# Performance work log

Measured on AMD Instinct MI355X. Metric: run time of the kernel, lower is better.

Reference implementation:

```python
import jax, jax.numpy as jnp
import numpy as np

N_NODES = 100000
N_EDGES = 1600000
INPUT_DIM = 128
HIDDEN = 128
OUTPUT_DIM = 2
NUM_LAYERS = 2
MAX_RECURSION = 10
TAU_THRESHOLD = 0.005


def setup_inputs() -> dict:
    key = jax.random.key(0)
    ks = jax.random.split(key, 16)
    s = 0.05
    x = jax.random.normal(ks[0], (N_NODES, INPUT_DIM), dtype=jnp.float32)
    edge_index = jax.random.randint(ks[1], (2, N_EDGES), 0, N_NODES, dtype=jnp.int64)
    W_in = jax.random.normal(ks[2], (HIDDEN, INPUT_DIM), dtype=jnp.float32) * s
    b_in = jax.random.normal(ks[3], (HIDDEN,), dtype=jnp.float32) * s
    Wd = jax.random.normal(ks[4], (NUM_LAYERS, HIDDEN, 2 * HIDDEN), dtype=jnp.float32) * s
    bd = jax.random.normal(ks[5], (NUM_LAYERS, HIDDEN), dtype=jnp.float32) * s
    Wt = jax.random.normal(ks[6], (1, HIDDEN), dtype=jnp.float32) * s
    bt = jax.random.normal(ks[7], (1,), dtype=jnp.float32) * s
    W_ih = jax.random.normal(ks[8], (3 * HIDDEN, HIDDEN), dtype=jnp.float32) * s
    W_hh = jax.random.normal(ks[9], (3 * HIDDEN, HIDDEN), dtype=jnp.float32) * s
    b_ih = jax.random.normal(ks[10], (3 * HIDDEN,), dtype=jnp.float32) * s
    b_hh = jax.random.normal(ks[11], (3 * HIDDEN,), dtype=jnp.float32) * s
    Wo = jax.random.normal(ks[12], (OUTPUT_DIM, HIDDEN), dtype=jnp.float32) * s
    bo = jax.random.normal(ks[13], (OUTPUT_DIM,), dtype=jnp.float32) * s
    return dict(x=x, edge_index=edge_index, W_in=W_in, b_in=b_in, Wd=Wd, bd=bd,
                Wt=Wt, bt=bt, W_ih=W_ih, W_hh=W_hh, b_ih=b_ih, b_hh=b_hh, Wo=Wo, bo=bo)


def _gru_cell(x, h, W_ih, W_hh, b_ih, b_hh):
    # torch.nn.GRUCell math
    gi = x @ W_ih.T + b_ih  # [N, 3H]
    gh = h @ W_hh.T + b_hh
    i_r, i_z, i_n = jnp.split(gi, 3, axis=-1)
    h_r, h_z, h_n = jnp.split(gh, 3, axis=-1)
    r = jax.nn.sigmoid(i_r + h_r)
    z = jax.nn.sigmoid(i_z + h_z)
    n = jnp.tanh(i_n + r * h_n)
    return (1.0 - z) * n + z * h


def reference(x, edge_index, W_in, b_in, Wd, bd, Wt, bt, W_ih, W_hh, b_ih, b_hh, Wo, bo):
    N = x.shape[0]
    row, col = edge_index[0], edge_index[1]
    h = jax.nn.relu(x @ W_in.T + b_in)  # [N, H]
    tau = None
    for l in range(NUM_LAYERS):
        diff = jnp.abs(h[row] - h[col])  # [E, H]
        diff_agg = jax.ops.segment_sum(diff, row, num_segments=N)  # [N, H]
        h = jax.nn.relu(jnp.concatenate([h, diff_agg], axis=-1) @ Wd[l].T + bd[l])
        tau = jax.nn.softplus(h @ Wt.T + bt).squeeze(-1)  # [N]
        # n_updates = clamp(floor(1/tau), max=MAX_RECURSION); node updated iff
        # n_updates > 0 and tau < TAU_THRESHOLD. The original inner loop applies
        # gru(diff_agg[i], h[i]) with the ORIGINAL h[i] each iteration, so repeated
        # application is idempotent -> single masked GRU step is exact same math.
        n_updates = jnp.minimum(jnp.floor(1.0 / tau).astype(jnp.int32), MAX_RECURSION)
        mask = (n_updates > 0) & (tau < TAU_THRESHOLD)
        h_gru = _gru_cell(diff_agg, h, W_ih, W_hh, b_ih, b_hh)
        h = jnp.where(mask[:, None], h_gru, h)
    out = h @ Wo.T + bo  # [N, OUTPUT_DIM]
    return out, tau
```

## Files before the change

### kernel.cpp

```cpp
#include <hip/hip_runtime.h>
#include <cstdint>
#include <cstddef>

#define HID 128
#define BSHIFT 7
#define NSB 256
#define MAXB 4096

__global__ __launch_bounds__(256)
void ecount_kernel(const int* __restrict__ row, int* __restrict__ countsT,
                   int E, int nbuck,
                   const float* __restrict__ W_in, const float* __restrict__ Wd,
                   const float* __restrict__ W_ih, const float* __restrict__ W_hh,
                   float* __restrict__ WinT, float* __restrict__ WdT0,
                   float* __restrict__ WdT1, float* __restrict__ WihT,
                   float* __restrict__ WhhT) {
  for (int i = blockIdx.x * 256 + threadIdx.x; i < 180224; i += NSB * 256) {
    int j = i;
    if (j < 16384) { int r = j >> 7, c = j & 127; WinT[c * 128 + r] = W_in[j]; continue; }
    j -= 16384;
    if (j < 32768) { int r = j >> 8, c = j & 255; WdT0[c * 128 + r] = Wd[j]; continue; }
    j -= 32768;
    if (j < 32768) { int r = j >> 8, c = j & 255; WdT1[c * 128 + r] = Wd[32768 + j]; continue; }
    j -= 32768;
    if (j < 49152) { int r = j >> 7, c = j & 127; WihT[c * 384 + r] = W_ih[j]; continue; }
    j -= 49152;
    { int r = j >> 7, c = j & 127; WhhT[c * 384 + r] = W_hh[j]; }
  }
  __shared__ int lh[1024];
  int b = blockIdx.x;
  for (int i = threadIdx.x; i < nbuck; i += 256) lh[i] = 0;
  __syncthreads();
  int per = (E + NSB - 1) / NSB;
  int s = b * per, e = min(s + per, E);
  for (int i = s + (int)threadIdx.x; i < e; i += 256)
    atomicAdd(&lh[row[i] >> BSHIFT], 1);
  __syncthreads();
  for (int i = threadIdx.x; i < nbuck; i += 256) countsT[i * NSB + b] = lh[i];
}

__global__ __launch_bounds__(NSB)
void bprefix_kernel(int* __restrict__ countsT, int* __restrict__ btotal, int nbuck) {
  __shared__ int sd[NSB];
  int bk = blockIdx.x;
  int t = threadIdx.x;
  int v = countsT[bk * NSB + t];
  sd[t] = v;
  __syncthreads();
  for (int off = 1; off < NSB; off <<= 1) {
    int u = (t >= off) ? sd[t - off] : 0;
    __syncthreads();
    sd[t] += u;
    __syncthreads();
  }
  countsT[bk * NSB + t] = sd[t] - v;
  if (t == NSB - 1) btotal[bk] = sd[t];
}

__global__ __launch_bounds__(1024)
void bstart_kernel(const int* __restrict__ btotal, int* __restrict__ bstart,
                   int* __restrict__ offsets, int N, int nbuck) {
  __shared__ int sd[1024];
  int t = threadIdx.x;
  int v = (t < nbuck) ? btotal[t] : 0;
  sd[t] = v;
  __syncthreads();
  for (int off = 1; off < 1024; off <<= 1) {
    int u = (t >= off) ? sd[t - off] : 0;
    __syncthreads();
    sd[t] += u;
    __syncthreads();
  }
  if (t < nbuck) bstart[t] = sd[t] - v;
  if (t == nbuck - 1) { bstart[nbuck] = sd[t]; offsets[N] = sd[t]; }
}

__global__ __launch_bounds__(256)
void escatter_kernel(const int* __restrict__ row, const int* __restrict__ col,
                     const int* __restrict__ countsT, const int* __restrict__ bstart,
                     int2* __restrict__ ebuf, int E, int nbuck) {
  __shared__ int lcur[1024];
  int b = blockIdx.x;
  for (int i = threadIdx.x; i < nbuck; i += 256)
    lcur[i] = bstart[i] + countsT[i * NSB + b];
  __syncthreads();
  int per = (E + NSB - 1) / NSB;
  int s = b * per, e = min(s + per, E);
  for (int i = s + (int)threadIdx.x; i < e; i += 256) {
    int r = row[i], c = col[i];
    int pos = atomicAdd(&lcur[r >> BSHIFT], 1);
    ebuf[pos] = make_int2(r, c);
  }
}

__global__ __launch_bounds__(256)
void bsort_kernel(const int2* __restrict__ ebuf, const int* __restrict__ bstart,
                  int* __restrict__ offsets, int* __restrict__ csr_col,
                  int N, int nbuck) {
  __shared__ int cnt[128], off[128], cur[128];
  __shared__ int lcol[MAXB];
  int bk = blockIdx.x;
  int tid = threadIdx.x;
  int s = bstart[bk], e = bstart[bk + 1];
  int m = e - s;
  if (tid < 128) cnt[tid] = 0;
  __syncthreads();
  for (int i = s + tid; i < e; i += 256)
    atomicAdd(&cnt[ebuf[i].x & 127], 1);
  __syncthreads();
  if (tid < 128) off[tid] = cnt[tid];
  __syncthreads();
  for (int d = 1; d < 128; d <<= 1) {
    int v = 0;
    if (tid < 128 && tid >= d) v = off[tid - d];
    __syncthreads();
    if (tid < 128) off[tid] += v;
    __syncthreads();
  }
  if (tid < 128) {
    cur[tid] = off[tid] - cnt[tid];
    int node = (bk << BSHIFT) + tid;
    if (node < N) offsets[node] = s + off[tid] - cnt[tid];
  }
  __syncthreads();
  if (m <= MAXB) {
    for (int i = s + tid; i < e; i += 256) {
      int2 rc = ebuf[i];
      int pos = atomicAdd(&cur[rc.x & 127], 1);
      lcol[pos] = rc.y;
    }
    __syncthreads();
    if (tid < 128) {
      int b0 = off[tid] - cnt[tid], b1 = off[tid];
      for (int i = b0 + 1; i < b1; ++i) {
        int key = lcol[i];
        int j = i - 1;
        while (j >= b0 && lcol[j] > key) { lcol[j + 1] = lcol[j]; --j; }
        lcol[j + 1] = key;
      }
    }
    __syncthreads();
    for (int i = tid; i < m; i += 256) csr_col[s + i] = lcol[i];
  } else {
    for (int i = s + tid; i < e; i += 256) {
      int2 rc = ebuf[i];
      int pos = atomicAdd(&cur[rc.x & 127], 1);
      csr_col[s + pos] = rc.y;
    }
  }
}

__global__ __launch_bounds__(256)
void aggregate_kernel(const float* __restrict__ h, const int* __restrict__ offsets,
                      const int* __restrict__ csr_col, float* __restrict__ diff,
                      int N) {
  int wave = threadIdx.x >> 6;
  int lane = threadIdx.x & 63;
  int node = blockIdx.x * 4 + wave;
  if (node >= N) return;
  int start = offsets[node], end = offsets[node + 1];
  int deg = end - start;
  const float2* hrow = (const float2*)(h + (size_t)node * HID);
  float2 hv = hrow[lane];
  float a0 = 0.f, a1 = 0.f;

  int batch = min(deg, 64);
  int myc = (lane < batch) ? csr_col[start + lane] : 0;
  int j = 0;
  for (; j + 16 <= batch; j += 16) {
    const float2* p0 = (const float2*)(h + (size_t)__shfl(myc, j + 0) * HID);
    const float2* p1 = (const float2*)(h + (size_t)__shfl(myc, j + 1) * HID);
    const float2* p2 = (const float2*)(h + (size_t)__shfl(myc, j + 2) * HID);
    const float2* p3 = (const float2*)(h + (size_t)__shfl(myc, j + 3) * HID);
    const float2* p4 = (const float2*)(h + (size_t)__shfl(myc, j + 4) * HID);
    const float2* p5 = (const float2*)(h + (size_t)__shfl(myc, j + 5) * HID);
    const float2* p6 = (const float2*)(h + (size_t)__shfl(myc, j + 6) * HID);
    const float2* p7 = (const float2*)(h + (size_t)__shfl(myc, j + 7) * HID);
    const float2* q0 = (const float2*)(h + (size_t)__shfl(myc, j + 8) * HID);
    const float2* q1 = (const float2*)(h + (size_t)__shfl(myc, j + 9) * HID);
    const float2* q2 = (const float2*)(h + (size_t)__shfl(myc, j + 10) * HID);
    const float2* q3 = (const float2*)(h + (size_t)__shfl(myc, j + 11) * HID);
    const float2* q4 = (const float2*)(h + (size_t)__shfl(myc, j + 12) * HID);
    const float2* q5 = (const float2*)(h + (size_t)__shfl(myc, j + 13) * HID);
    const float2* q6 = (const float2*)(h + (size_t)__shfl(myc, j + 14) * HID);
    const float2* q7 = (const float2*)(h + (size_t)__shfl(myc, j + 15) * HID);
    float2 x0 = p0[lane], x1 = p1[lane], x2 = p2[lane], x3 = p3[lane];
    float2 x4 = p4[lane], x5 = p5[lane], x6 = p6[lane], x7 = p7[lane];
    float2 y0 = q0[lane], y1 = q1[lane], y2 = q2[lane], y3 = q3[lane];
    float2 y4 = q4[lane], y5 = q5[lane], y6 = q6[lane], y7 = q7[lane];
    a0 += fabsf(hv.x - x0.x) + fabsf(hv.x - x1.x) + fabsf(hv.x - x2.x) + fabsf(hv.x - x3.x)
        + fabsf(hv.x - x4.x) + fabsf(hv.x - x5.x) + fabsf(hv.x - x6.x) + fabsf(hv.x - x7.x);
    a1 += fabsf(hv.y - x0.y) + fabsf(hv.y - x1.y) + fabsf(hv.y - x2.y) + fabsf(hv.y - x3.y)
        + fabsf(hv.y - x4.y) + fabsf(hv.y - x5.y) + fabsf(hv.y - x6.y) + fabsf(hv.y - x7.y);
    a0 += fabsf(hv.x - y0.x) + fabsf(hv.x - y1.x) + fabsf(hv.x - y2.x) + fabsf(hv.x - y3.x)
        + fabsf(hv.x - y4.x) + fabsf(hv.x - y5.x) + fabsf(hv.x - y6.x) + fabsf(hv.x - y7.x);
    a1 += fabsf(hv.y - y0.y) + fabsf(hv.y - y1.y) + fabsf(hv.y - y2.y) + fabsf(hv.y - y3.y)
        + fabsf(hv.y - y4.y) + fabsf(hv.y - y5.y) + fabsf(hv.y - y6.y) + fabsf(hv.y - y7.y);
  }
  for (; j + 8 <= batch; j += 8) {
    const float2* p0 = (const float2*)(h + (size_t)__shfl(myc, j + 0) * HID);
    const float2* p1 = (const float2*)(h + (size_t)__shfl(myc, j + 1) * HID);
    const float2* p2 = (const float2*)(h + (size_t)__shfl(myc, j + 2) * HID);
    const float2* p3 = (const float2*)(h + (size_t)__shfl(myc, j + 3) * HID);
    const float2* p4 = (const float2*)(h + (size_t)__shfl(myc, j + 4) * HID);
    const float2* p5 = (const float2*)(h + (size_t)__shfl(myc, j + 5) * HID);
    const float2* p6 = (const float2*)(h + (size_t)__shfl(myc, j + 6) * HID);
    const float2* p7 = (const float2*)(h + (size_t)__shfl(myc, j + 7) * HID);
    float2 x0 = p0[lane], x1 = p1[lane], x2 = p2[lane], x3 = p3[lane];
    float2 x4 = p4[lane], x5 = p5[lane], x6 = p6[lane], x7 = p7[lane];
    a0 += fabsf(hv.x - x0.x) + fabsf(hv.x - x1.x) + fabsf(hv.x - x2.x) + fabsf(hv.x - x3.x)
        + fabsf(hv.x - x4.x) + fabsf(hv.x - x5.x) + fabsf(hv.x - x6.x) + fabsf(hv.x - x7.x);
    a1 += fabsf(hv.y - x0.y) + fabsf(hv.y - x1.y) + fabsf(hv.y - x2.y) + fabsf(hv.y - x3.y)
        + fabsf(hv.y - x4.y) + fabsf(hv.y - x5.y) + fabsf(hv.y - x6.y) + fabsf(hv.y - x7.y);
  }
  for (; j < batch; ++j) {
    const float2* p = (const float2*)(h + (size_t)__shfl(myc, j) * HID);
    float2 x = p[lane];
    a0 += fabsf(hv.x - x.x);
    a1 += fabsf(hv.y - x.y);
  }
  for (int e = start + 64; e < end; ++e) {
    const float2* p = (const float2*)(h + (size_t)csr_col[e] * HID);
    float2 x = p[lane];
    a0 += fabsf(hv.x - x.x);
    a1 += fabsf(hv.y - x.y);
  }
  *(float2*)(diff + (size_t)node * HID + 2 * lane) = make_float2(a0, a1);
}

template<bool TAU>
__global__ __launch_bounds__(256)
void gemm_kernel(const float* __restrict__ A1, const float* __restrict__ A2,
                 const float* __restrict__ BT, const float* __restrict__ bias,
                 float* __restrict__ C, int M, int nchunks,
                 const float* __restrict__ Wt, const float* __restrict__ bt,
                 float* __restrict__ tau_out, int* __restrict__ mlist,
                 int* __restrict__ mcount) {
  __shared__ float As[32][68];
  __shared__ float Bs[32][128];
  __shared__ float taured[64];
  int tid = threadIdx.x;
  int tx = tid & 31;
  int ty = tid >> 5;
  int i0 = blockIdx.x * 64;
  float acc[8][4] = {};

  for (int kc = 0; kc < nchunks; ++kc) {
    const float* A = (kc < 4) ? A1 : A2;
    int ksrc = (kc & 3) * 32;
    int kglob = kc * 32;
    #pragma unroll
    for (int q = 0; q < 2; ++q) {
      int f = q * 256 + tid;
      int i = f >> 3;
      int kq = (f & 7) << 2;
      int ig = i0 + i; if (ig >= M) ig = M - 1;
      float4 v = *(const float4*)(A + (size_t)ig * HID + ksrc + kq);
      As[kq + 0][i] = v.x; As[kq + 1][i] = v.y;
      As[kq + 2][i] = v.z; As[kq + 3][i] = v.w;
    }
    #pragma unroll
    for (int q = 0; q < 4; ++q) {
      int f = q * 256 + tid;
      int k = f >> 5; int c4 = (f & 31) << 2;
      *(float4*)&Bs[k][c4] = *(const float4*)(BT + (size_t)(kglob + k) * HID + c4);
    }
    __syncthreads();
    #pragma unroll
    for (int k = 0; k < 32; ++k) {
      float a[8];
      const float4* ap = (const float4*)&As[k][ty * 8];
      float4 a0 = ap[0], a1 = ap[1];
      a[0]=a0.x; a[1]=a0.y; a[2]=a0.z; a[3]=a0.w;
      a[4]=a1.x; a[5]=a1.y; a[6]=a1.z; a[7]=a1.w;
      float4 b4 = *(const float4*)&Bs[k][tx * 4];
      #pragma unroll
      for (int r = 0; r < 8; ++r) {
        acc[r][0] = fmaf(a[r], b4.x, acc[r][0]);
        acc[r][1] = fmaf(a[r], b4.y, acc[r][1]);
        acc[r][2] = fmaf(a[r], b4.z, acc[r][2]);
        acc[r][3] = fmaf(a[r], b4.w, acc[r][3]);
      }
    }
    __syncthreads();
  }

  float4 bias4 = *(const float4*)(bias + tx * 4);
  float bias_r[4] = {bias4.x, bias4.y, bias4.z, bias4.w};
  float wt_r[4] = {0.f, 0.f, 0.f, 0.f};
  if constexpr (TAU) {
    float4 w4 = *(const float4*)(Wt + tx * 4);
    wt_r[0] = w4.x; wt_r[1] = w4.y; wt_r[2] = w4.z; wt_r[3] = w4.w;
  }
  #pragma unroll
  for (int r = 0; r < 8; ++r) {
    int row = i0 + ty * 8 + r;
    bool ok = row < M;
    float v0 = fmaxf(acc[r][0] + bias_r[0], 0.f);
    float v1 = fmaxf(acc[r][1] + bias_r[1], 0.f);
    float v2 = fmaxf(acc[r][2] + bias_r[2], 0.f);
    float v3 = fmaxf(acc[r][3] + bias_r[3], 0.f);
    if (ok) {
      float4 v4 = make_float4(v0, v1, v2, v3);
      *(float4*)(C + (size_t)row * HID + tx * 4) = v4;
    }
    if constexpr (TAU) {
      float p = v0 * wt_r[0];
      p = fmaf(v1, wt_r[1], p);
      p = fmaf(v2, wt_r[2], p);
      p = fmaf(v3, wt_r[3], p);
      p += __shfl_down(p, 16, 32);
      p += __shfl_down(p, 8, 32);
      p += __shfl_down(p, 4, 32);
      p += __shfl_down(p, 2, 32);
      p += __shfl_down(p, 1, 32);
      if (tx == 0) taured[ty * 8 + r] = p;
    }
  }
  if constexpr (TAU) {
    __syncthreads();
    if (tid < 64) {
      int row = i0 + tid;
      if (row < M) {
        float pre = taured[tid] + bt[0];
        float tau = (pre > 20.f) ? pre : log1pf(expf(pre));
        tau_out[row] = tau;
        if (tau < 0.005f && (1.0f / tau) < 2147483648.0f) {
          int pos = atomicAdd(mcount, 1);
          mlist[pos] = row;
        }
      }
    }
  }
}

__global__ __launch_bounds__(512)
void gru_kernel(const float* __restrict__ diff, float* __restrict__ h,
                const int* __restrict__ list, const int* __restrict__ count,
                const float* __restrict__ WihT, const float* __restrict__ WhhT,
                const float* __restrict__ b_ih, const float* __restrict__ b_hh) {
  int cnt = *count;
  int base = blockIdx.x * 32;
  if (base >= cnt) return;
  __shared__ float dl[32][HID];
  __shared__ float hl[32][HID];
  __shared__ int ids[32];
  int tid = threadIdx.x;
  if (tid < 32) ids[tid] = (base + tid < cnt) ? list[base + tid] : -1;
  __syncthreads();
  #pragma unroll
  for (int q = 0; q < 8; ++q) {
    int f = q * 512 + tid;
    int r = f >> 7, c = f & 127;
    int id = ids[r];
    int src = (id >= 0) ? id : 0;
    dl[r][c] = diff[(size_t)src * HID + c];
    hl[r][c] = h[(size_t)src * HID + c];
  }
  __syncthreads();
  int tx = tid & 127, ty = tid >> 7;
  float air[8] = {}, aiz[8] = {}, ain[8] = {}, ahr[8] = {}, ahz[8] = {}, ahn[8] = {};
  for (int k = 0; k < HID; ++k) {
    float wir = WihT[k * 384 + tx];
    float wiz = WihT[k * 384 + 128 + tx];
    float win = WihT[k * 384 + 256 + tx];
    float whr = WhhT[k * 384 + tx];
    float whz = WhhT[k * 384 + 128 + tx];
    float whn = WhhT[k * 384 + 256 + tx];
    #pragma unroll
    for (int r = 0; r < 8; ++r) {
      float dk = dl[ty * 8 + r][k];
      float hk = hl[ty * 8 + r][k];
      air[r] = fmaf(dk, wir, air[r]);
      aiz[r] = fmaf(dk, wiz, aiz[r]);
      ain[r] = fmaf(dk, win, ain[r]);
      ahr[r] = fmaf(hk, whr, ahr[r]);
      ahz[r] = fmaf(hk, whz, ahz[r]);
      ahn[r] = fmaf(hk, whn, ahn[r]);
    }
  }
  float bir = b_ih[tx], biz = b_ih[128 + tx], bin = b_ih[256 + tx];
  float bhr = b_hh[tx], bhz = b_hh[128 + tx], bhn = b_hh[256 + tx];
  #pragma unroll
  for (int r = 0; r < 8; ++r) {
    int id = ids[ty * 8 + r];
    if (id < 0) continue;
    float rg = 1.f / (1.f + expf(-((air[r] + bir) + (ahr[r] + bhr))));
    float z  = 1.f / (1.f + expf(-((aiz[r] + biz) + (ahz[r] + bhz))));
    float n  = tanhf((ain[r] + bin) + rg * (ahn[r] + bhn));
    float hv = hl[ty * 8 + r][tx];
    h[(size_t)id * HID + tx] = (1.f - z) * n + z * hv;
  }
}

__global__ void out_kernel(const float* __restrict__ h, const float* __restrict__ Wo,
                           const float* __restrict__ bo, float* __restrict__ out, int N) {
  int g = blockIdx.x * blockDim.x + threadIdx.x;
  int node = g >> 5;
  int sub = threadIdx.x & 31;
  if (node >= N) return;
  float4 hv = *(const float4*)(h + (size_t)node * HID + sub * 4);
  float4 w0 = *(const float4*)(Wo + sub * 4);
  float4 w1 = *(const float4*)(Wo + 128 + sub * 4);
  float s0 = hv.x * w0.x + hv.y * w0.y + hv.z * w0.z + hv.w * w0.w;
  float s1 = hv.x * w1.x + hv.y * w1.y + hv.z * w1.z + hv.w * w1.w;
  for (int d = 16; d; d >>= 1) {
    s0 += __shfl_down(s0, d, 32);
    s1 += __shfl_down(s1, d, 32);
  }
  if (sub == 0) {
    out[(size_t)node * 2 + 0] = s0 + bo[0];
    out[(size_t)node * 2 + 1] = s1 + bo[1];
  }
}

extern "C" void kernel_launch(void* const* d_in, const int* in_sizes, int n_in,
                              void* d_out, int out_size, void* d_ws, size_t ws_size,
                              hipStream_t stream) {
  const float* x    = (const float*)d_in[0];
  const int*   ei   = (const int*)d_in[1];
  const float* W_in = (const float*)d_in[2];
  const float* b_in = (const float*)d_in[3];
  const float* Wd   = (const float*)d_in[4];
  const float* bd   = (const float*)d_in[5];
  const float* Wt   = (const float*)d_in[6];
  const float* bt   = (const float*)d_in[7];
  const float* W_ih = (const float*)d_in[8];
  const float* W_hh = (const float*)d_in[9];
  const float* b_ih = (const float*)d_in[10];
  const float* b_hh = (const float*)d_in[11];
  const float* Wo   = (const float*)d_in[12];
  const float* bo   = (const float*)d_in[13];

  const int N = in_sizes[0] / HID;
  const int E = in_sizes[1] / 2;
  const int* rowp = ei;
  const int* colp = ei + E;
  const int nbuck = (N + (1 << BSHIFT) - 1) >> BSHIFT;

  char* p = (char*)d_ws;
  auto alloc = [&](size_t bytes) { void* r = (void*)p; p += (bytes + 255) & ~(size_t)255; return r; };
  float* hA     = (float*)alloc((size_t)N * HID * 4);
  float* hB     = (float*)alloc((size_t)N * HID * 4);
  float* diff   = (float*)alloc((size_t)N * HID * 4);
  float* WinT   = (float*)alloc(128 * 128 * 4);
  float* WdT0   = (float*)alloc(256 * 128 * 4);
  float* WdT1   = (float*)alloc(256 * 128 * 4);
  float* WihT   = (float*)alloc(128 * 384 * 4);
  float* WhhT   = (float*)alloc(128 * 384 * 4);
  float* tau0   = (float*)alloc((size_t)N * 4);
  int*   list   = (int*)alloc((size_t)N * 4);
  int*   count  = (int*)alloc(256);
  int*   countsT= (int*)alloc((size_t)1024 * NSB * 4);
  int*   btotal = (int*)alloc(1024 * 4);
  int*   bstart = (int*)alloc(1028 * 4);
  int*   offs   = (int*)alloc(((size_t)N + 1) * 4);
  int*   csrcol = (int*)alloc((size_t)E * 4);
  int2*  ebuf   = (int2*)alloc((size_t)E * 8);

  float* out_ptr = (float*)d_out;
  float* tau_out = (float*)d_out + (size_t)N * 2;

  hipMemsetAsync(count, 0, 8, stream);

  ecount_kernel<<<NSB, 256, 0, stream>>>(rowp, countsT, E, nbuck,
                                         W_in, Wd, W_ih, W_hh,
                                         WinT, WdT0, WdT1, WihT, WhhT);
  bprefix_kernel<<<nbuck, NSB, 0, stream>>>(countsT, btotal, nbuck);
  bstart_kernel<<<1, 1024, 0, stream>>>(btotal, bstart, offs, N, nbuck);
  escatter_kernel<<<NSB, 256, 0, stream>>>(rowp, colp, countsT, bstart, ebuf, E, nbuck);
  bsort_kernel<<<nbuck, 256, 0, stream>>>(ebuf, bstart, offs, csrcol, N, nbuck);

  const int gemm_blocks = (N + 63) / 64;
  const int agg_blocks = (N + 3) / 4;
  const int gru_blocks = (N + 31) / 32;

  gemm_kernel<false><<<gemm_blocks, 256, 0, stream>>>(
      x, nullptr, WinT, b_in, hA, N, 4, nullptr, nullptr, nullptr, nullptr, nullptr);

  aggregate_kernel<<<agg_blocks, 256, 0, stream>>>(hA, offs, csrcol, diff, N);
  gemm_kernel<true><<<gemm_blocks, 256, 0, stream>>>(
      hA, diff, WdT0, bd, hB, N, 8, Wt, bt, tau0, list, count);
  gru_kernel<<<gru_blocks, 512, 0, stream>>>(diff, hB, list, count, WihT, WhhT, b_ih, b_hh);

  aggregate_kernel<<<agg_blocks, 256, 0, stream>>>(hB, offs, csrcol, diff, N);
  gemm_kernel<true><<<gemm_blocks, 256, 0, stream>>>(
      hB, diff, WdT1, bd + 128, hA, N, 8, Wt, bt, tau_out, list, count + 1);
  gru_kernel<<<gru_blocks, 512, 0, stream>>>(diff, hA, list, count + 1, WihT, WhhT, b_ih, b_hh);

  out_kernel<<<((size_t)N * 32 + 255) / 256, 256, 0, stream>>>(hA, Wo, bo, out_ptr, N);
}
```

Measured before the change: 742.3 us.

## Fuse neighbor abs-diff aggregation into the dense layer GEMM kernel

Removes the separate aggregate kernel and computes each 64-row block's diff aggregation at the start of the GEMM block. Each wave aggregates 16 nodes in sequence, writes the results to global memory, and then a fence and barrier make them visible before the GEMM reads them. This saves a kernel launch and lets the diff rows be read back while still cache-hot. In exchange, the aggregation now runs at only 4 waves per 64 nodes in sequence, with the 16-wide unroll dropped, which lowers memory-level parallelism for the gather-bound phase.

Result: slower. 1.110 ms (+49.5%).

```diff
diff --git a/kernel.cpp b/kernel.cpp
--- a/kernel.cpp
+++ b/kernel.cpp
@@ -150,92 +150,16 @@
   }
 }
 
+template<bool TAU, bool AGG>
 __global__ __launch_bounds__(256)
-void aggregate_kernel(const float* __restrict__ h, const int* __restrict__ offsets,
-                      const int* __restrict__ csr_col, float* __restrict__ diff,
-                      int N) {
-  int wave = threadIdx.x >> 6;
-  int lane = threadIdx.x & 63;
-  int node = blockIdx.x * 4 + wave;
-  if (node >= N) return;
-  int start = offsets[node], end = offsets[node + 1];
-  int deg = end - start;
-  const float2* hrow = (const float2*)(h + (size_t)node * HID);
-  float2 hv = hrow[lane];
-  float a0 = 0.f, a1 = 0.f;
-
-  int batch = min(deg, 64);
-  int myc = (lane < batch) ? csr_col[start + lane] : 0;
-  int j = 0;
-  for (; j + 16 <= batch; j += 16) {
-    const float2* p0 = (const float2*)(h + (size_t)__shfl(myc, j + 0) * HID);
-    const float2* p1 = (const float2*)(h + (size_t)__shfl(myc, j + 1) * HID);
-    const float2* p2 = (const float2*)(h + (size_t)__shfl(myc, j + 2) * HID);
-    const float2* p3 = (const float2*)(h + (size_t)__shfl(myc, j + 3) * HID);
-    const float2* p4 = (const float2*)(h + (size_t)__shfl(myc, j + 4) * HID);
-    const float2* p5 = (const float2*)(h + (size_t)__shfl(myc, j + 5) * HID);
-    const float2* p6 = (const float2*)(h + (size_t)__shfl(myc, j + 6) * HID);
-    const float2* p7 = (const float2*)(h + (size_t)__shfl(myc, j + 7) * HID);
-    const float2* q0 = (const float2*)(h + (size_t)__shfl(myc, j + 8) * HID);
-    const float2* q1 = (const float2*)(h + (size_t)__shfl(myc, j + 9) * HID);
-    const float2* q2 = (const float2*)(h + (size_t)__shfl(myc, j + 10) * HID);
-    const float2* q3 = (const float2*)(h + (size_t)__shfl(myc, j + 11) * HID);
-    const float2* q4 = (const float2*)(h + (size_t)__shfl(myc, j + 12) * HID);
-    const float2* q5 = (const float2*)(h + (size_t)__shfl(myc, j + 13) * HID);
-    const float2* q6 = (const float2*)(h + (size_t)__shfl(myc, j + 14) * HID);
-    const float2* q7 = (const float2*)(h + (size_t)__shfl(myc, j + 15) * HID);
-    float2 x0 = p0[lane], x1 = p1[lane], x2 = p2[lane], x3 = p3[lane];
-    float2 x4 = p4[lane], x5 = p5[lane], x6 = p6[lane], x7 = p7[lane];
-    float2 y0 = q0[lane], y1 = q1[lane], y2 = q2[lane], y3 = q3[lane];
-    float2 y4 = q4[lane], y5 = q5[lane], y6 = q6[lane], y7 = q7[lane];
-    a0 += fabsf(hv.x - x0.x) + fabsf(hv.x - x1.x) + fabsf(hv.x - x2.x) + fabsf(hv.x - x3.x)
-        + fabsf(hv.x - x4.x) + fabsf(hv.x - x5.x) + fabsf(hv.x - x6.x) + fabsf(hv.x - x7.x);
-    a1 += fabsf(hv.y - x0.y) + fabsf(hv.y - x1.y) + fabsf(hv.y - x2.y) + fabsf(hv.y - x3.y)
-        + fabsf(hv.y - x4.y) + fabsf(hv.y - x5.y) + fabsf(hv.y - x6.y) + fabsf(hv.y - x7.y);
-    a0 += fabsf(hv.x - y0.x) + fabsf(hv.x - y1.x) + fabsf(hv.x - y2.x) + fabsf(hv.x - y3.x)
-        + fabsf(hv.x - y4.x) + fabsf(hv.x - y5.x) + fabsf(hv.x - y6.x) + fabsf(hv.x - y7.x);
-    a1 += fabsf(hv.y - y0.y) + fabsf(hv.y - y1.y) + fabsf(hv.y - y2.y) + fabsf(hv.y - y3.y)
-        + fabsf(hv.y - y4.y) + fabsf(hv.y - y5.y) + fabsf(hv.y - y6.y) + fabsf(hv.y - y7.y);
-  }
-  for (; j + 8 <= batch; j += 8) {
-    const float2* p0 = (const float2*)(h + (size_t)__shfl(myc, j + 0) * HID);
-    const float2* p1 = (const float2*)(h + (size_t)__shfl(myc, j + 1) * HID);
-    const float2* p2 = (const float2*)(h + (size_t)__shfl(myc, j + 2) * HID);
-    const float2* p3 = (const float2*)(h + (size_t)__shfl(myc, j + 3) * HID);
-    const float2* p4 = (const float2*)(h + (size_t)__shfl(myc, j + 4) * HID);
-    const float2* p5 = (const float2*)(h + (size_t)__shfl(myc, j + 5) * HID);
-    const float2* p6 = (const float2*)(h + (size_t)__shfl(myc, j + 6) * HID);
-    const float2* p7 = (const float2*)(h + (size_t)__shfl(myc, j + 7) * HID);
-    float2 x0 = p0[lane], x1 = p1[lane], x2 = p2[lane], x3 = p3[lane];
-    float2 x4 = p4[lane], x5 = p5[lane], x6 = p6[lane], x7 = p7[lane];
-    a0 += fabsf(hv.x - x0.x) + fabsf(hv.x - x1.x) + fabsf(hv.x - x2.x) + fabsf(hv.x - x3.x)
-        + fabsf(hv.x - x4.x) + fabsf(hv.x - x5.x) + fabsf(hv.x - x6.x) + fabsf(hv.x - x7.x);
-    a1 += fabsf(hv.y - x0.y) + fabsf(hv.y - x1.y) + fabsf(hv.y - x2.y) + fabsf(hv.y - x3.y)
-        + fabsf(hv.y - x4.y) + fabsf(hv.y - x5.y) + fabsf(hv.y - x6.y) + fabsf(hv.y - x7.y);
-  }
-  for (; j < batch; ++j) {
-    const float2* p = (const float2*)(h + (size_t)__shfl(myc, j) * HID);
-    float2 x = p[lane];
-    a0 += fabsf(hv.x - x.x);
-    a1 += fabsf(hv.y - x.y);
-  }
-  for (int e = start + 64; e < end; ++e) {
-    const float2* p = (const float2*)(h + (size_t)csr_col[e] * HID);
-    float2 x = p[lane];
-    a0 += fabsf(hv.x - x.x);
-    a1 += fabsf(hv.y - x.y);
-  }
-  *(float2*)(diff + (size_t)node * HID + 2 * lane) = make_float2(a0, a1);
-}
-
-template<bool TAU>
-__global__ __launch_bounds__(256)
-void gemm_kernel(const float* __restrict__ A1, const float* __restrict__ A2,
+void gemm_kernel(const float* __restrict__ A1, const float* A2,
                  const float* __restrict__ BT, const float* __restrict__ bias,
                  float* __restrict__ C, int M, int nchunks,
                  const float* __restrict__ Wt, const float* __restrict__ bt,
                  float* __restrict__ tau_out, int* __restrict__ mlist,
-                 int* __restrict__ mcount) {
+                 int* __restrict__ mcount,
+                 const int* __restrict__ offsets, const int* __restrict__ csr_col,
+                 float* D ) {
   __shared__ float As[32][68];
   __shared__ float Bs[32][128];
   __shared__ float taured[64];
@@ -243,8 +167,56 @@
   int tx = tid & 31;
   int ty = tid >> 5;
   int i0 = blockIdx.x * 64;
+
+  if constexpr (AGG) {
+    int wave = tid >> 6;
+    int lane = tid & 63;
+    for (int t = 0; t < 16; ++t) {
+      int node = i0 + (wave << 4) + t;
+      if (node >= M) break;
+      int start = offsets[node], end = offsets[node + 1];
+      int deg = end - start;
+      const float2* hrow = (const float2*)(A1 + (size_t)node * HID);
+      float2 hv = hrow[lane];
+      float a0 = 0.f, a1 = 0.f;
+      int batch = min(deg, 64);
+      int myc = (lane < batch) ? csr_col[start + lane] : 0;
+      int j = 0;
+      for (; j + 8 <= batch; j += 8) {
+        const float2* p0 = (const float2*)(A1 + (size_t)__shfl(myc, j + 0) * HID);
+        const float2* p1 = (const float2*)(A1 + (size_t)__shfl(myc, j + 1) * HID);
+        const float2* p2 = (const float2*)(A1 + (size_t)__shfl(myc, j + 2) * HID);
+        const float2* p3 = (const float2*)(A1 + (size_t)__shfl(myc, j + 3) * HID);
+        const float2* p4 = (const float2*)(A1 + (size_t)__shfl(myc, j + 4) * HID);
+        const float2* p5 = (const float2*)(A1 + (size_t)__shfl(myc, j + 5) * HID);
+        const float2* p6 = (const float2*)(A1 + (size_t)__shfl(myc, j + 6) * HID);
+        const float2* p7 = (const float2*)(A1 + (size_t)__shfl(myc, j + 7) * HID);
+        float2 x0 = p0[lane], x1 = p1[lane], x2 = p2[lane], x3 = p3[lane];
+        float2 x4 = p4[lane], x5 = p5[lane], x6 = p6[lane], x7 = p7[lane];
+        a0 += fabsf(hv.x - x0.x) + fabsf(hv.x - x1.x) + fabsf(hv.x - x2.x) + fabsf(hv.x - x3.x)
+            + fabsf(hv.x - x4.x) + fabsf(hv.x - x5.x) + fabsf(hv.x - x6.x) + fabsf(hv.x - x7.x);
+        a1 += fabsf(hv.y - x0.y) + fabsf(hv.y - x1.y) + fabsf(hv.y - x2.y) + fabsf(hv.y - x3.y)
+            + fabsf(hv.y - x4.y) + fabsf(hv.y - x5.y) + fabsf(hv.y - x6.y) + fabsf(hv.y - x7.y);
+      }
+      for (; j < batch; ++j) {
+        const float2* p = (const float2*)(A1 + (size_t)__shfl(myc, j) * HID);
+        float2 x = p[lane];
+        a0 += fabsf(hv.x - x.x);
+        a1 += fabsf(hv.y - x.y);
+      }
+      for (int e = start + 64; e < end; ++e) {
+        const float2* p = (const float2*)(A1 + (size_t)csr_col[e] * HID);
+        float2 x = p[lane];
+        a0 += fabsf(hv.x - x.x);
+        a1 += fabsf(hv.y - x.y);
+      }
+      *(float2*)(D + (size_t)node * HID + 2 * lane) = make_float2(a0, a1);
+    }
+    __threadfence();
+    __syncthreads();
+  }
+
   float acc[8][4] = {};
-
   for (int kc = 0; kc < nchunks; ++kc) {
     const float* A = (kc < 4) ? A1 : A2;
     int ksrc = (kc & 3) * 32;
@@ -472,20 +444,20 @@
   bsort_kernel<<<nbuck, 256, 0, stream>>>(ebuf, bstart, offs, csrcol, N, nbuck);
 
   const int gemm_blocks = (N + 63) / 64;
-  const int agg_blocks = (N + 3) / 4;
   const int gru_blocks = (N + 31) / 32;
 
-  gemm_kernel<false><<<gemm_blocks, 256, 0, stream>>>(
-      x, nullptr, WinT, b_in, hA, N, 4, nullptr, nullptr, nullptr, nullptr, nullptr);
-
-  aggregate_kernel<<<agg_blocks, 256, 0, stream>>>(hA, offs, csrcol, diff, N);
-  gemm_kernel<true><<<gemm_blocks, 256, 0, stream>>>(
-      hA, diff, WdT0, bd, hB, N, 8, Wt, bt, tau0, list, count);
+  gemm_kernel<false, false><<<gemm_blocks, 256, 0, stream>>>(
+      x, nullptr, WinT, b_in, hA, N, 4, nullptr, nullptr, nullptr, nullptr, nullptr,
+      nullptr, nullptr, nullptr);
+
+  gemm_kernel<true, true><<<gemm_blocks, 256, 0, stream>>>(
+      hA, diff, WdT0, bd, hB, N, 8, Wt, bt, tau0, list, count,
+      offs, csrcol, diff);
   gru_kernel<<<gru_blocks, 512, 0, stream>>>(diff, hB, list, count, WihT, WhhT, b_ih, b_hh);
 
-  aggregate_kernel<<<agg_blocks, 256, 0, stream>>>(hB, offs, csrcol, diff, N);
-  gemm_kernel<true><<<gemm_blocks, 256, 0, stream>>>(
-      hB, diff, WdT1, bd + 128, hA, N, 8, Wt, bt, tau_out, list, count + 1);
+  gemm_kernel<true, true><<<gemm_blocks, 256, 0, stream>>>(
+      hB, diff, WdT1, bd + 128, hA, N, 8, Wt, bt, tau_out, list, count + 1,
+      offs, csrcol, diff);
   gru_kernel<<<gru_blocks, 512, 0, stream>>>(diff, hA, list, count + 1, WihT, WhhT, b_ih, b_hh);
 
   out_kernel<<<((size_t)N * 32 + 255) / 256, 256, 0, stream>>>(hA, Wo, bo, out_ptr, N);
```
